# Kernel optimization log

Hardware: AMD Instinct MI355X
Metric: run time of the kernel (lower is better)

The kernel has to match this reference:

```python
import jax, jax.numpy as jnp
import numpy as np

D_MODEL = 1024
NUM_HEADS = 16
D_K = D_MODEL // NUM_HEADS


def setup_inputs() -> dict:
    key = jax.random.key(0)
    k1, k2, k3, k4 = jax.random.split(key, 4)
    scale = 1.0 / np.sqrt(D_MODEL)
    inp = {
        "input": jax.random.normal(k1, (2, 2048, D_MODEL), dtype=jnp.float32),
        "W_qkv": jax.random.normal(k2, (D_MODEL, 3 * D_MODEL), dtype=jnp.float32) * scale,
        "b_qkv": jax.random.normal(k3, (3 * D_MODEL,), dtype=jnp.float32) * 0.02,
        "W_out": jax.random.normal(k4, (D_MODEL, D_MODEL), dtype=jnp.float32) * scale,
    }
    return inp


def reference(input, W_qkv, b_qkv, W_out):
    B, S, _ = input.shape
    qkv = input @ W_qkv + b_qkv                      # [B,S,3D]
    q, k, v = jnp.split(qkv, 3, axis=-1)             # each [B,S,D]
    def heads(x):
        return x.reshape(B, S, NUM_HEADS, D_K).transpose(0, 2, 1, 3)  # [B,H,S,dk]
    q, k, v = heads(q), heads(k), heads(v)
    scores = jnp.einsum("bhsd,bhtd->bhst", q, k) / jnp.sqrt(jnp.float32(D_K))
    attn = jax.nn.softmax(scores, axis=-1)           # [B,H,S,S]
    out = jnp.einsum("bhst,bhtd->bhsd", attn, v)     # [B,H,S,dk]
    out = out.transpose(0, 2, 1, 3).reshape(B, S, D_MODEL)
    return out @ W_out
```

## Files before the change

### kernel.cpp

```cpp
#include <hip/hip_runtime.h>

typedef unsigned short u16;
typedef unsigned int u32;
typedef __attribute__((ext_vector_type(8))) short short8;
typedef __attribute__((ext_vector_type(8))) __bf16 bf16x8;
typedef __attribute__((ext_vector_type(4))) float f32x4;
typedef __attribute__((ext_vector_type(16))) float f32x16;

__device__ __forceinline__ u16 f2bf(float f) {
  union { float f; u32 u; } c; c.f = f;
  u32 u = c.u + 0x7fffu + ((c.u >> 16) & 1u);
  return (u16)(u >> 16);
}
__device__ __forceinline__ f32x4 mfma16(short8 a, short8 b, f32x4 c) {
  return __builtin_amdgcn_mfma_f32_16x16x32_bf16(
      __builtin_bit_cast(bf16x8, a), __builtin_bit_cast(bf16x8, b), c, 0, 0, 0);
}
__device__ __forceinline__ f32x16 mfma32(short8 a, short8 b, f32x16 c) {
  return __builtin_amdgcn_mfma_f32_32x32x16_bf16(
      __builtin_bit_cast(bf16x8, a), __builtin_bit_cast(bf16x8, b), c, 0, 0, 0);
}
__device__ __forceinline__ float fexp2(float x) {
  float r; asm("v_exp_f32 %0, %1" : "=v"(r) : "v"(x)); return r;
}
__device__ __forceinline__ void gl16(const u16* g, u16* l) {
  __builtin_amdgcn_global_load_lds(
      (const __attribute__((address_space(1))) unsigned*)g,
      (__attribute__((address_space(3))) unsigned*)l, 16, 0, 0);
}

__global__ __launch_bounds__(256) void transpose_f32_bf16(const float* __restrict__ in,
                                                          u16* __restrict__ out,
                                                          int R, int C) {
  __shared__ u16 tile[32][33];
  int tx = threadIdx.x & 31, ty = threadIdx.x >> 5;
  int c0 = blockIdx.x * 32, r0 = blockIdx.y * 32;
  for (int i = 0; i < 32; i += 8)
    tile[ty + i][tx] = f2bf(in[(size_t)(r0 + ty + i) * C + c0 + tx]);
  __syncthreads();
  for (int i = 0; i < 32; i += 8)
    out[(size_t)(c0 + ty + i) * R + r0 + tx] = tile[tx][ty + i];
}

template <int MODE>
__global__ __launch_bounds__(256) void gemm_bt(const void* __restrict__ Av,
                                               const void* __restrict__ Bv,
                                               const float* __restrict__ bias,
                                               void* __restrict__ C0v,
                                               void* __restrict__ C1v,
                                               int M, int N, int K) {
  __shared__ __align__(16) u16 As[2][9216];
  __shared__ __align__(16) u16 Bs[2][9216];
  const int tid = threadIdx.x;
  const int w = tid >> 6, l = tid & 63;
  const int i16 = l & 15, q4 = l >> 4;

  const int nbx = gridDim.x;
  const int nwg = nbx * gridDim.y;
  int fid = blockIdx.y * nbx + blockIdx.x;
  int wg = (nwg & 7) ? fid : ((fid & 7) * (nwg >> 3) + (fid >> 3));
  const int m0 = (wg / nbx) * 128, n0 = (wg % nbx) * 128;
  const int wm = (w >> 1) * 64, wn = (w & 1) * 64;

  const int arow = tid >> 3, akg = (tid & 7) * 8;

  const u16* A16p = (const u16*)Av;
  const u16* B16p = (const u16*)Bv;
  const float* Fp = (MODE == 1) ? (const float*)Av : (const float*)Bv;
  const int fbase = (MODE == 1) ? m0 : n0;

  f32x4 acc[4][4] = {};
  float4 pf[4][2];

#define STAGE_A16(bufi, kk) {                                                  \
    _Pragma("unroll") for (int i = 0; i < 4; ++i) {                            \
      const int s = w * 4 + i;                                                 \
      gl16(&A16p[(size_t)(m0 + (s >> 1) * 16 + i16) * K + (kk) + (s & 1) * 32  \
                 + q4 * 8],                                                    \
           &As[bufi][s * 512]); } }
#define STAGE_B16(bufi, kk) {                                                  \
    _Pragma("unroll") for (int i = 0; i < 4; ++i) {                            \
      const int s = w * 4 + i;                                                 \
      gl16(&B16p[(size_t)(n0 + (s >> 1) * 16 + i16) * K + (kk) + (s & 1) * 32  \
                 + q4 * 8],                                                    \
           &Bs[bufi][s * 512]); } }
#define LOAD_PFX(kk) {                                                         \
    _Pragma("unroll") for (int i = 0; i < 4; ++i) {                            \
      const float* src = Fp + (size_t)(fbase + arow + i * 32) * K + (kk) + akg;\
      pf[i][0] = *(const float4*)src;                                          \
      pf[i][1] = *(const float4*)(src + 4); } }
#define CVT_X(bufi) {                                                          \
    _Pragma("unroll") for (int i = 0; i < 4; ++i) {                            \
      short8 v;                                                                \
      v[0] = (short)f2bf(pf[i][0].x); v[1] = (short)f2bf(pf[i][0].y);          \
      v[2] = (short)f2bf(pf[i][0].z); v[3] = (short)f2bf(pf[i][0].w);          \
      v[4] = (short)f2bf(pf[i][1].x); v[5] = (short)f2bf(pf[i][1].y);          \
      v[6] = (short)f2bf(pf[i][1].z); v[7] = (short)f2bf(pf[i][1].w);          \
      u16* d = (MODE == 1) ? &As[bufi][(arow + i * 32) * 72 + akg]             \
                           : &Bs[bufi][(arow + i * 32) * 72 + akg];            \
      *(short8*)d = v; } }

  const int nk = K >> 6;
  if constexpr (MODE == 0) {
    STAGE_A16(0, 0); STAGE_B16(0, 0);
  } else if constexpr (MODE == 1) {
    LOAD_PFX(0); STAGE_B16(0, 0); CVT_X(0); LOAD_PFX(64);
  } else {
    LOAD_PFX(0); STAGE_A16(0, 0); CVT_X(0); LOAD_PFX(64);
  }
  __syncthreads();

  for (int t = 0; t < nk; ++t) {
    const int cur = t & 1, nxt = cur ^ 1;
    const int k1 = (t + 1) << 6;
    if (t + 1 < nk) {
      if constexpr (MODE == 0) {
        STAGE_A16(nxt, k1); STAGE_B16(nxt, k1);
      } else if constexpr (MODE == 1) {
        STAGE_B16(nxt, k1); CVT_X(nxt);
        if (t + 2 < nk) LOAD_PFX(k1 + 64);
      } else {
        STAGE_A16(nxt, k1); CVT_X(nxt);
        if (t + 2 < nk) LOAD_PFX(k1 + 64);
      }
    }
#pragma unroll
    for (int ks = 0; ks < 2; ++ks) {
      short8 af[4], bfr[4];
#pragma unroll
      for (int mi = 0; mi < 4; ++mi) {
        if constexpr (MODE == 1)
          af[mi] = *(short8*)&As[cur][(wm + mi * 16 + i16) * 72 + ks * 32 + q4 * 8];
        else
          af[mi] = *(short8*)((char*)&As[cur][0] +
                              (((wm >> 4) + mi) * 2 + ks) * 1024 + l * 16);
      }
#pragma unroll
      for (int ni = 0; ni < 4; ++ni) {
        if constexpr (MODE == 2)
          bfr[ni] = *(short8*)&Bs[cur][(wn + ni * 16 + i16) * 72 + ks * 32 + q4 * 8];
        else
          bfr[ni] = *(short8*)((char*)&Bs[cur][0] +
                               (((wn >> 4) + ni) * 2 + ks) * 1024 + l * 16);
      }
#pragma unroll
      for (int mi = 0; mi < 4; ++mi)
#pragma unroll
        for (int ni = 0; ni < 4; ++ni)
          acc[mi][ni] = mfma16(af[mi], bfr[ni], acc[mi][ni]);
    }
    __syncthreads();
  }
#undef STAGE_A16
#undef STAGE_B16
#undef LOAD_PFX
#undef CVT_X

  if constexpr (MODE == 0) {
    float* dstf = (float*)C0v;
    for (int mi = 0; mi < 4; ++mi) {
      int row = m0 + wm + mi * 16 + q4 * 4;
      for (int ni = 0; ni < 4; ++ni) {
        int nl = wn + ni * 16 + i16;
        for (int r = 0; r < 4; ++r)
          dstf[(size_t)(row + r) * N + n0 + nl] = acc[mi][ni][r];
      }
    }
  } else if constexpr (MODE == 1) {
    u16* dstb; int cb;
    if (n0 < 1024) { dstb = (u16*)C0v; cb = n0; }
    else           { dstb = (u16*)C1v; cb = n0 - 1024; }
    for (int mi = 0; mi < 4; ++mi) {
      int row = m0 + wm + mi * 16 + q4 * 4;
      for (int ni = 0; ni < 4; ++ni) {
        int nl = wn + ni * 16 + i16;
        float b = bias[n0 + nl];
        for (int r = 0; r < 4; ++r)
          dstb[(size_t)(row + r) * 1024 + cb + nl] = f2bf(acc[mi][ni][r] + b);
      }
    }
  } else {
    u16* dstb = (u16*)C0v + ((n0 >= 2048) ? (size_t)1024 * 2048 : 0);
    const int cb = n0 & 2047;
    for (int mi = 0; mi < 4; ++mi) {
      int row = m0 + wm + mi * 16 + q4 * 4;
      float4 bv = *(const float4*)&bias[row];
      const float bvr[4] = {bv.x, bv.y, bv.z, bv.w};
      for (int ni = 0; ni < 4; ++ni) {
        int nl = wn + ni * 16 + i16;
        for (int r = 0; r < 4; ++r)
          dstb[(size_t)(row + r) * 2048 + cb + nl] = f2bf(acc[mi][ni][r] + bvr[r]);
      }
    }
  }
}

__global__ __launch_bounds__(512, 4) void attn_flash(u16* __restrict__ Qbuf,
                                                     const u16* __restrict__ Kall,
                                                     const u16* __restrict__ VTall) {
  constexpr float CSC = 0.18033688011112042f;
  constexpr float MC  = 96.0f * CSC;
  __shared__ __align__(16) u16 SH[32768];
  __shared__ float RsumB[128], RsumT[128];

  const int tid = threadIdx.x;
  const int w = tid >> 6, l = tid & 63;
  const int l31 = l & 31, hi = l >> 5;
  const int qg = w >> 1, th = w & 1;

  u16* KsL = SH + th * 16384;
  u16* VsL = SH + th * 16384 + 8192;

  const int L = blockIdx.x;
  const int xcd = L & 7, rr = L >> 3;
  const int qb = rr & 15, gg = rr >> 4;
  const int g = gg * 8 + xcd;
  const int h = g & 15, bat = g >> 4;
  const int q0 = qb * 128;

  u16* Q = Qbuf + (size_t)bat * 2048 * 1024;
  const u16* Kb = Kall + (size_t)bat * 2048 * 1024;
  const u16* Vtb = VTall + (size_t)bat * 1024 * 2048;

  short8 qf[4];
  {
    const u16* qrow = Q + (size_t)(q0 + qg * 32 + l31) * 1024 + h * 64 + hi * 8;
#pragma unroll
    for (int ks = 0; ks < 4; ++ks) qf[ks] = *(const short8*)(qrow + ks * 16);
  }

  const u16* Ksrc = Kb + (size_t)((qg & 1) * 32 + l31) * 1024 + h * 64 +
                    (qg >> 1) * 16 + hi * 8;
  const u16* Vsrc = Vtb + (size_t)(h * 64 + (qg & 1) * 32 + l31) * 2048 +
                    (qg >> 1) * 16 + hi * 8;
  const int tbase = th * 1024;

#define STAGE(buf_, t0_) {                                                   \
    const size_t tk = (size_t)(t0_) * 1024;                                  \
    gl16(Ksrc + tk,      KsL + (buf_) * 4096 + qg * 512);                    \
    gl16(Ksrc + tk + 32, KsL + (buf_) * 4096 + (qg + 4) * 512);              \
    gl16(Vsrc + (t0_),      VsL + (buf_) * 4096 + qg * 512);                 \
    gl16(Vsrc + (t0_) + 32, VsL + (buf_) * 4096 + (qg + 4) * 512); }

  f32x16 o0 = {}, o1 = {};
  float sm0 = 0.f, sm1 = 0.f, sm2 = 0.f, sm3 = 0.f;

  STAGE(0, tbase);
  __syncthreads();

  for (int i = 0; i < 16; ++i) {
    const int cur = i & 1;
    if (i + 1 < 16) STAGE(cur ^ 1, tbase + (i + 1) * 64);

    const char* Kc = (const char*)KsL + cur * 8192 + l * 16;
    const char* Vc = (const char*)VsL + cur * 8192 + l * 16;

    f32x16 st0 = {}, st1 = {};
#pragma unroll
    for (int ks = 0; ks < 4; ++ks) {
      short8 kf0 = *(const short8*)(Kc + ks * 2048);
      short8 kf1 = *(const short8*)(Kc + ks * 2048 + 1024);
      st0 = mfma32(kf0, qf[ks], st0);
      st1 = mfma32(kf1, qf[ks], st1);
    }

    u32 W[16];
#define SOFTMAX_PACK(stt, WB) {                                             \
      float p_[16];                                                         \
      _Pragma("unroll") for (int r = 0; r < 16; ++r)                        \
          p_[r] = fexp2(__builtin_fmaf(stt[r], CSC, -MC));                  \
      _Pragma("unroll") for (int r = 0; r < 16; r += 4) {                   \
        sm0 += p_[r]; sm1 += p_[r + 1]; sm2 += p_[r + 2]; sm3 += p_[r + 3]; \
      }                                                                     \
      _Pragma("unroll") for (int m = 0; m < 4; ++m)                         \
        _Pragma("unroll") for (int s = 0; s < 2; ++s)                       \
          asm("v_cvt_pk_bf16_f32 %0, %1, %2"                                \
              : "=v"(W[(WB) + m * 2 + s])                                   \
              : "v"(p_[4 * m + 2 * s]), "v"(p_[4 * m + 2 * s + 1]));        \
    }
    SOFTMAX_PACK(st0, 0)
    SOFTMAX_PACK(st1, 8)
#undef SOFTMAX_PACK

#pragma unroll
    for (int u = 0; u < 4; ++u) {
      const int base = (u >> 1) * 8 + (u & 1) * 4;
      u32 a0 = W[base], a1 = W[base + 1], b0 = W[base + 2], b1 = W[base + 3];
      asm("v_permlane32_swap_b32 %0, %1" : "+v"(a0), "+v"(b0));
      asm("v_permlane32_swap_b32 %0, %1" : "+v"(a1), "+v"(b1));
      int4 af4;
      af4.x = (int)a0; af4.y = (int)a1; af4.z = (int)b0; af4.w = (int)b1;
      const short8 pfr = __builtin_bit_cast(short8, af4);
      const short8 vf0 = *(const short8*)(Vc + u * 2048);
      const short8 vf1 = *(const short8*)(Vc + u * 2048 + 1024);
      o0 = mfma32(pfr, vf0, o0);
      o1 = mfma32(pfr, vf1, o1);
    }
    __syncthreads();
  }
#undef STAGE

  float rs = (sm0 + sm1) + (sm2 + sm3);
  rs += __shfl_xor(rs, 32);
  __syncthreads();
  float* MF = (float*)SH;
  if (th == 1) {
    float* dst = MF + (qg * 64 + l) * 36;
    *(f32x16*)dst = o0;
    *(f32x16*)(dst + 16) = o1;
    if (hi == 0) RsumB[qg * 32 + l31] = rs;
  }
  __syncthreads();
  if (th == 0) {
    const float* src = MF + (qg * 64 + l) * 36;
    o0 += *(const f32x16*)src;
    o1 += *(const f32x16*)(src + 16);
    float rtot = rs + RsumB[qg * 32 + l31];
    if (hi == 0) RsumT[qg * 32 + l31] = rtot;
  }
  __syncthreads();
  if (th == 0) {
#pragma unroll
    for (int r = 0; r < 16; ++r) {
      const int qq = (r & 3) + 8 * (r >> 2) + 4 * hi;
      const float inv = 1.0f / RsumT[qg * 32 + qq];
      u16* dst = Q + (size_t)(q0 + qg * 32 + qq) * 1024 + h * 64 + l31;
      dst[0]  = f2bf(o0[r] * inv);
      dst[32] = f2bf(o1[r] * inv);
    }
  }
}

extern "C" void kernel_launch(void* const* d_in, const int* in_sizes, int n_in,
                              void* d_out, int out_size, void* d_ws, size_t ws_size,
                              hipStream_t stream) {
  const float* X    = (const float*)d_in[0];
  const float* Wqkv = (const float*)d_in[1];
  const float* bqkv = (const float*)d_in[2];
  const float* Wout = (const float*)d_in[3];

  u16* Qbuf = (u16*)d_out;
  u16* WT1  = Qbuf + (size_t)4096 * 1024;
  u16* WT2  = WT1 + (size_t)3072 * 1024;
  u16* Kbuf = (u16*)d_ws;
  u16* VT   = Kbuf + (size_t)4096 * 1024;
  float* Cws = (float*)d_ws;

  transpose_f32_bf16<<<dim3(96, 32), 256, 0, stream>>>(Wqkv, WT1, 1024, 3072);
  transpose_f32_bf16<<<dim3(32, 32), 256, 0, stream>>>(Wout, WT2, 1024, 1024);

  gemm_bt<1><<<dim3(16, 32), 256, 0, stream>>>(
      X, WT1, bqkv, Qbuf, Kbuf, 4096, 2048, 1024);

  gemm_bt<2><<<dim3(32, 8), 256, 0, stream>>>(
      WT1 + (size_t)2048 * 1024, X, bqkv + 2048, VT, nullptr, 1024, 4096, 1024);

  attn_flash<<<dim3(512), 512, 0, stream>>>(Qbuf, Kbuf, VT);

  gemm_bt<0><<<dim3(8, 32), 256, 0, stream>>>(
      Qbuf, WT2, nullptr, Cws, nullptr, 4096, 1024, 1024);

  hipMemcpyAsync(d_out, Cws, (size_t)4096 * 1024 * sizeof(float),
                 hipMemcpyDeviceToDevice, stream);
}
```

Measured before the change: 228.0 us.

## Write K and V in attention-tiled layout; halve M-tile for V and output GEMMs

The QKV GEMM epilogues now scatter K and V^T directly into a per-(batch, head, 64-token block) tiled layout that matches the attention kernel's LDS staging order. Each attention staging load then becomes a contiguous 4096-element chunk instead of a strided gather. Separately, the GEMM is templated on BM, and the V-projection and output-projection GEMMs use 64-row tiles to launch twice as many workgroups. The costs are scattered, less coalesced epilogue stores and lower per-tile data reuse in the smaller-tile GEMMs.

```diff
diff --git a/kernel.cpp b/kernel.cpp
--- a/kernel.cpp
+++ b/kernel.cpp
@@ -28,6 +28,7 @@
       (const __attribute__((address_space(1))) unsigned*)g,
       (__attribute__((address_space(3))) unsigned*)l, 16, 0, 0);
 }
+
 
 __global__ __launch_bounds__(256) void transpose_f32_bf16(const float* __restrict__ in,
                                                           u16* __restrict__ out,
@@ -42,15 +43,19 @@
     out[(size_t)(c0 + ty + i) * R + r0 + tx] = tile[tx][ty + i];
 }
 
-template <int MODE>
+template <int MODE, int BM>
 __global__ __launch_bounds__(256) void gemm_bt(const void* __restrict__ Av,
                                                const void* __restrict__ Bv,
                                                const float* __restrict__ bias,
                                                void* __restrict__ C0v,
                                                void* __restrict__ C1v,
                                                int M, int N, int K) {
-  __shared__ __align__(16) u16 As[2][9216];
-  __shared__ __align__(16) u16 Bs[2][9216];
+  constexpr int MI  = BM / 32;
+  constexpr int NSA = BM / 8;
+  constexpr int ASZ = (MODE == 1) ? 9216 : NSA * 512;
+  constexpr int BSZ = (MODE == 2) ? 9216 : 8192;
+  __shared__ __align__(16) u16 As[2][ASZ];
+  __shared__ __align__(16) u16 Bs[2][BSZ];
   const int tid = threadIdx.x;
   const int w = tid >> 6, l = tid & 63;
   const int i16 = l & 15, q4 = l >> 4;
@@ -59,8 +64,8 @@
   const int nwg = nbx * gridDim.y;
   int fid = blockIdx.y * nbx + blockIdx.x;
   int wg = (nwg & 7) ? fid : ((fid & 7) * (nwg >> 3) + (fid >> 3));
-  const int m0 = (wg / nbx) * 128, n0 = (wg % nbx) * 128;
-  const int wm = (w >> 1) * 64, wn = (w & 1) * 64;
+  const int m0 = (wg / nbx) * BM, n0 = (wg % nbx) * 128;
+  const int wm = (w >> 1) * (BM / 2), wn = (w & 1) * 64;
 
   const int arow = tid >> 3, akg = (tid & 7) * 8;
 
@@ -69,12 +74,12 @@
   const float* Fp = (MODE == 1) ? (const float*)Av : (const float*)Bv;
   const int fbase = (MODE == 1) ? m0 : n0;
 
-  f32x4 acc[4][4] = {};
+  f32x4 acc[MI][4] = {};
   float4 pf[4][2];
 
 #define STAGE_A16(bufi, kk) {                                                  \
-    _Pragma("unroll") for (int i = 0; i < 4; ++i) {                            \
-      const int s = w * 4 + i;                                                 \
+    _Pragma("unroll") for (int i = 0; i < NSA / 4; ++i) {                      \
+      const int s = w * (NSA / 4) + i;                                         \
       gl16(&A16p[(size_t)(m0 + (s >> 1) * 16 + i16) * K + (kk) + (s & 1) * 32  \
                  + q4 * 8],                                                    \
            &As[bufi][s * 512]); } }
@@ -126,9 +131,9 @@
     }
 #pragma unroll
     for (int ks = 0; ks < 2; ++ks) {
-      short8 af[4], bfr[4];
-#pragma unroll
-      for (int mi = 0; mi < 4; ++mi) {
+      short8 af[MI], bfr[4];
+#pragma unroll
+      for (int mi = 0; mi < MI; ++mi) {
         if constexpr (MODE == 1)
           af[mi] = *(short8*)&As[cur][(wm + mi * 16 + i16) * 72 + ks * 32 + q4 * 8];
         else
@@ -144,7 +149,7 @@
                                (((wn >> 4) + ni) * 2 + ks) * 1024 + l * 16);
       }
 #pragma unroll
-      for (int mi = 0; mi < 4; ++mi)
+      for (int mi = 0; mi < MI; ++mi)
 #pragma unroll
         for (int ni = 0; ni < 4; ++ni)
           acc[mi][ni] = mfma16(af[mi], bfr[ni], acc[mi][ni]);
@@ -158,7 +163,7 @@
 
   if constexpr (MODE == 0) {
     float* dstf = (float*)C0v;
-    for (int mi = 0; mi < 4; ++mi) {
+    for (int mi = 0; mi < MI; ++mi) {
       int row = m0 + wm + mi * 16 + q4 * 4;
       for (int ni = 0; ni < 4; ++ni) {
         int nl = wn + ni * 16 + i16;
@@ -167,29 +172,59 @@
       }
     }
   } else if constexpr (MODE == 1) {
-    u16* dstb; int cb;
-    if (n0 < 1024) { dstb = (u16*)C0v; cb = n0; }
-    else           { dstb = (u16*)C1v; cb = n0 - 1024; }
-    for (int mi = 0; mi < 4; ++mi) {
-      int row = m0 + wm + mi * 16 + q4 * 4;
-      for (int ni = 0; ni < 4; ++ni) {
-        int nl = wn + ni * 16 + i16;
-        float b = bias[n0 + nl];
-        for (int r = 0; r < 4; ++r)
-          dstb[(size_t)(row + r) * 1024 + cb + nl] = f2bf(acc[mi][ni][r] + b);
+    if (n0 < 1024) {
+      u16* dstb = (u16*)C0v;
+      for (int mi = 0; mi < MI; ++mi) {
+        int row = m0 + wm + mi * 16 + q4 * 4;
+        for (int ni = 0; ni < 4; ++ni) {
+          int nl = wn + ni * 16 + i16;
+          float b = bias[n0 + nl];
+          for (int r = 0; r < 4; ++r)
+            dstb[(size_t)(row + r) * 1024 + n0 + nl] = f2bf(acc[mi][ni][r] + b);
+        }
+      }
+    } else {
+      u16* KT = (u16*)C1v;
+      for (int mi = 0; mi < MI; ++mi) {
+        int row = m0 + wm + mi * 16 + q4 * 4;
+        for (int ni = 0; ni < 4; ++ni) {
+          int nl = wn + ni * 16 + i16;
+          const int d = (n0 - 1024) + nl;
+          const int hh = d >> 6, dh = d & 63;
+          const int sd = (dh >> 4) << 1;
+          const int lh = ((dh >> 3) & 1) << 5;
+          const int j = dh & 7;
+          float b = bias[n0 + nl];
+          for (int r = 0; r < 4; ++r) {
+            const int tok = row + r;
+            const int bb = tok >> 11, t = tok & 2047;
+            size_t addr = ((size_t)((bb << 4) + hh) * 32 + (t >> 6)) * 4096
+                        + (sd + ((t >> 5) & 1)) * 512 + (lh + (t & 31)) * 8 + j;
+            KT[addr] = f2bf(acc[mi][ni][r] + b);
+          }
+        }
       }
     }
   } else {
-    u16* dstb = (u16*)C0v + ((n0 >= 2048) ? (size_t)1024 * 2048 : 0);
-    const int cb = n0 & 2047;
-    for (int mi = 0; mi < 4; ++mi) {
-      int row = m0 + wm + mi * 16 + q4 * 4;
-      float4 bv = *(const float4*)&bias[row];
+    u16* VTt = (u16*)C0v;
+    for (int mi = 0; mi < MI; ++mi) {
+      int drow = m0 + wm + mi * 16 + q4 * 4;
+      float4 bv = *(const float4*)&bias[drow];
       const float bvr[4] = {bv.x, bv.y, bv.z, bv.w};
       for (int ni = 0; ni < 4; ++ni) {
-        int nl = wn + ni * 16 + i16;
-        for (int r = 0; r < 4; ++r)
-          dstb[(size_t)(row + r) * 2048 + cb + nl] = f2bf(acc[mi][ni][r] + bvr[r]);
+        int col = n0 + wn + ni * 16 + i16;
+        const int bb = col >> 11, t = col & 2047;
+        const int su = ((t >> 4) & 3) << 1;
+        const int lt = ((t >> 3) & 1) << 5;
+        const int j = t & 7;
+        const size_t tb0 = ((size_t)(bb << 4) * 32 + (t >> 6)) * 4096;
+        for (int r = 0; r < 4; ++r) {
+          const int d = drow + r;
+          const int hh = d >> 6, dh = d & 63;
+          size_t addr = tb0 + (size_t)hh * 131072
+                      + (su + (dh >> 5)) * 512 + (lt + (dh & 31)) * 8 + j;
+          VTt[addr] = f2bf(acc[mi][ni][r] + bvr[r]);
+        }
       }
     }
   }
@@ -219,8 +254,8 @@
   const int q0 = qb * 128;
 
   u16* Q = Qbuf + (size_t)bat * 2048 * 1024;
-  const u16* Kb = Kall + (size_t)bat * 2048 * 1024;
-  const u16* Vtb = VTall + (size_t)bat * 1024 * 2048;
+  const u16* ksrc = Kall + (size_t)((bat << 4) + h) * 131072 + l * 8;
+  const u16* vsrc = VTall + (size_t)((bat << 4) + h) * 131072 + l * 8;
 
   short8 qf[4];
   {
@@ -229,28 +264,23 @@
     for (int ks = 0; ks < 4; ++ks) qf[ks] = *(const short8*)(qrow + ks * 16);
   }
 
-  const u16* Ksrc = Kb + (size_t)((qg & 1) * 32 + l31) * 1024 + h * 64 +
-                    (qg >> 1) * 16 + hi * 8;
-  const u16* Vsrc = Vtb + (size_t)(h * 64 + (qg & 1) * 32 + l31) * 2048 +
-                    (qg >> 1) * 16 + hi * 8;
-  const int tbase = th * 1024;
-
-#define STAGE(buf_, t0_) {                                                   \
-    const size_t tk = (size_t)(t0_) * 1024;                                  \
-    gl16(Ksrc + tk,      KsL + (buf_) * 4096 + qg * 512);                    \
-    gl16(Ksrc + tk + 32, KsL + (buf_) * 4096 + (qg + 4) * 512);              \
-    gl16(Vsrc + (t0_),      VsL + (buf_) * 4096 + qg * 512);                 \
-    gl16(Vsrc + (t0_) + 32, VsL + (buf_) * 4096 + (qg + 4) * 512); }
+#define STAGE(buf_, it_) {                                                   \
+    const size_t toff = (size_t)(it_) * 4096;                                \
+    gl16(ksrc + toff + qg * 512,       KsL + (buf_) * 4096 + qg * 512);      \
+    gl16(ksrc + toff + (qg + 4) * 512, KsL + (buf_) * 4096 + (qg + 4) * 512);\
+    gl16(vsrc + toff + qg * 512,       VsL + (buf_) * 4096 + qg * 512);      \
+    gl16(vsrc + toff + (qg + 4) * 512, VsL + (buf_) * 4096 + (qg + 4) * 512); }
 
   f32x16 o0 = {}, o1 = {};
   float sm0 = 0.f, sm1 = 0.f, sm2 = 0.f, sm3 = 0.f;
 
+  const int tbase = th * 16;
   STAGE(0, tbase);
   __syncthreads();
 
   for (int i = 0; i < 16; ++i) {
     const int cur = i & 1;
-    if (i + 1 < 16) STAGE(cur ^ 1, tbase + (i + 1) * 64);
+    if (i + 1 < 16) STAGE(cur ^ 1, tbase + i + 1);
 
     const char* Kc = (const char*)KsL + cur * 8192 + l * 16;
     const char* Vc = (const char*)VsL + cur * 8192 + l * 16;
@@ -349,15 +379,15 @@
   transpose_f32_bf16<<<dim3(96, 32), 256, 0, stream>>>(Wqkv, WT1, 1024, 3072);
   transpose_f32_bf16<<<dim3(32, 32), 256, 0, stream>>>(Wout, WT2, 1024, 1024);
 
-  gemm_bt<1><<<dim3(16, 32), 256, 0, stream>>>(
+  gemm_bt<1, 128><<<dim3(16, 32), 256, 0, stream>>>(
       X, WT1, bqkv, Qbuf, Kbuf, 4096, 2048, 1024);
 
-  gemm_bt<2><<<dim3(32, 8), 256, 0, stream>>>(
+  gemm_bt<2, 64><<<dim3(32, 16), 256, 0, stream>>>(
       WT1 + (size_t)2048 * 1024, X, bqkv + 2048, VT, nullptr, 1024, 4096, 1024);
 
   attn_flash<<<dim3(512), 512, 0, stream>>>(Qbuf, Kbuf, VT);
 
-  gemm_bt<0><<<dim3(8, 32), 256, 0, stream>>>(
+  gemm_bt<0, 64><<<dim3(8, 64), 256, 0, stream>>>(
       Qbuf, WT2, nullptr, Cws, nullptr, 4096, 1024, 1024);
 
   hipMemcpyAsync(d_out, Cws, (size_t)4096 * 1024 * sizeof(float),
```

Result: faster. 218.8 us (-4.0%).
